# Optimization experiments

Hardware: AMD Instinct MI355X
Metric: run time of the kernel (lower is better)

Reference implementation:

```python
import jax, jax.numpy as jnp
import numpy as np

B, S, D = 2, 2048, 2048          # batch, seq_len, model_dim
H, HD, RD, L = 16, 128, 64, 512  # heads, head_dim, rope_dim, latent_dim


def _rope_cos_sin(seq_len, dim, dtype):
    inv_freq = 1.0 / (10000.0 ** (jnp.arange(0, dim, 2, dtype=jnp.float32) / dim))
    freqs = jnp.outer(jnp.arange(seq_len, dtype=jnp.float32), inv_freq)  # [S, dim/2]
    emb = jnp.concatenate([freqs, freqs], axis=-1)                        # [S, dim]
    return jnp.cos(emb).astype(dtype), jnp.sin(emb).astype(dtype)


def _rotate_half(x):
    x1, x2 = jnp.split(x, 2, axis=-1)
    return jnp.concatenate([-x2, x1], axis=-1)


def _apply_rope(q, k):
    # q, k: [B, S, H, rope_dim]
    cos, sin = _rope_cos_sin(q.shape[1], q.shape[-1], q.dtype)
    cos = cos[None, :, None, :]
    sin = sin[None, :, None, :]
    return q * cos + _rotate_half(q) * sin, k * cos + _rotate_half(k) * sin


def setup_inputs() -> dict:
    key = jax.random.key(0)
    ks = jax.random.split(key, 6)
    x = jax.random.normal(ks[0], (B, S, D), dtype=jnp.float32)
    mask = jnp.tril(jnp.ones((1, 1, S, S), dtype=jnp.bool_))  # causal
    s = lambda fan_in: 1.0 / np.sqrt(fan_in)
    w_kv_down = jax.random.normal(ks[1], (D, L), jnp.float32) * s(D)
    w_kv_up = jax.random.normal(ks[2], (L, H * (2 * HD + RD)), jnp.float32) * s(L)
    w_q_down = jax.random.normal(ks[3], (D, L), jnp.float32) * s(D)
    w_q_up = jax.random.normal(ks[4], (L, H * (HD + RD)), jnp.float32) * s(L)
    w_o = jax.random.normal(ks[5], (H * HD, D), jnp.float32) * s(H * HD)
    return dict(x=x, mask=mask, w_kv_down=w_kv_down, w_kv_up=w_kv_up,
                w_q_down=w_q_down, w_q_up=w_q_up, w_o=w_o)


def reference(x, mask, w_kv_down, w_kv_up, w_q_down, w_q_up, w_o):
    b, s, _ = x.shape
    # low-rank KV path
    kv_full = (x @ w_kv_down @ w_kv_up).reshape(b, s, H, 2 * HD + RD)
    k_content = kv_full[..., :HD]
    k_rope = kv_full[..., HD:HD + RD]
    v = kv_full[..., HD + RD:]                     # [b, s, H, HD]
    # low-rank Q path
    q_full = (x @ w_q_down @ w_q_up).reshape(b, s, H, HD + RD)
    q_content = q_full[..., :HD]
    q_rope = q_full[..., HD:]
    # partial RoPE on the rope slice only
    q_rope, k_rope = _apply_rope(q_rope, k_rope)
    q = jnp.concatenate([q_content, q_rope], axis=-1)  # [b, s, H, HD+RD]
    k = jnp.concatenate([k_content, k_rope], axis=-1)
    scale = 1.0 / np.sqrt(HD + RD)
    scores = jnp.einsum('bqhd,bkhd->bhqk', q, k) * scale
    scores = jnp.where(mask, scores, jnp.finfo(scores.dtype).min)
    attn = jax.nn.softmax(scores, axis=-1)          # dropout_p=0.0 -> identity
    context = jnp.einsum('bhqk,bkhd->bqhd', attn, v).reshape(b, s, H * HD)
    return context @ w_o
```

## Files before the change

### kernel.cpp

```cpp
#include <hip/hip_runtime.h>
#include <hip/hip_bf16.h>

#define B_ 2
#define S_ 2048
#define D_ 2048
#define H_ 16
#define HD_ 128
#define RD_ 64
#define L_ 512
#define BS_ (B_ * S_)
#define KVH 320
#define QH 192

typedef unsigned short u16;
typedef __bf16 bf16x8 __attribute__((ext_vector_type(8)));
typedef float f32x4 __attribute__((ext_vector_type(4)));
typedef unsigned short us8 __attribute__((ext_vector_type(8)));
typedef unsigned short us4 __attribute__((ext_vector_type(4)));

#define MFMA16(A, B, C) __builtin_amdgcn_mfma_f32_16x16x32_bf16((A), (B), (C), 0, 0, 0)

__device__ __forceinline__ u16 f2bf(float f) {
    unsigned int u = __builtin_bit_cast(unsigned int, f);
    u += 0x7FFFu + ((u >> 16) & 1u);
    return (u16)(u >> 16);
}
__device__ __forceinline__ float bf2f(u16 u) {
    unsigned int x = ((unsigned int)u) << 16;
    return __builtin_bit_cast(float, x);
}
__device__ __forceinline__ void async16(const void* g, void* l) {
    __builtin_amdgcn_global_load_lds((void __attribute__((address_space(1)))*)g,
                                     (void __attribute__((address_space(3)))*)l, 16, 0, 0);
}
__device__ __forceinline__ int swz4(int row) { return (row + (row >> 2)) & 3; }

__global__ __launch_bounds__(256) void conv_f32_bf16(const float* __restrict__ in,
                                                     u16* __restrict__ outp) {
    const int i = blockIdx.x * 256 + threadIdx.x;
    float4 v = *(const float4*)(in + (size_t)i * 4);
    us4 o; o[0] = f2bf(v.x); o[1] = f2bf(v.y); o[2] = f2bf(v.z); o[3] = f2bf(v.w);
    *(us4*)(outp + (size_t)i * 4) = o;
}

__global__ __launch_bounds__(256) void transpose_f32_bf16(const float* __restrict__ W,
                                                          u16* __restrict__ Wt,
                                                          int K, int N) {
    __shared__ float tile[32][33];
    const int t = threadIdx.x, tx = t & 31, ty = t >> 5;
    const int n0 = blockIdx.x * 32, k0 = blockIdx.y * 32;
#pragma unroll
    for (int r = 0; r < 4; r++)
        tile[ty + 8 * r][tx] = W[(size_t)(k0 + ty + 8 * r) * N + n0 + tx];
    __syncthreads();
#pragma unroll
    for (int r = 0; r < 4; r++)
        Wt[(size_t)(n0 + ty + 8 * r) * K + k0 + tx] = f2bf(tile[tx][ty + 8 * r]);
}

__global__ __launch_bounds__(256) void transpose_v(const u16* __restrict__ kvf,
                                                   u16* __restrict__ vtg) {
    __shared__ u16 tile[32][33];
    const int t = threadIdx.x, tx = t & 31, ty = t >> 5;
    const int bh = blockIdx.z, b = bh >> 4, h = bh & 15;
    const int s0 = blockIdx.x * 32, d0 = blockIdx.y * 32;
#pragma unroll
    for (int r = 0; r < 4; r++)
        tile[ty + 8 * r][tx] = kvf[(size_t)(b * S_ + s0 + ty + 8 * r) * (H_ * KVH) + h * KVH + QH + d0 + tx];
    __syncthreads();
#pragma unroll
    for (int r = 0; r < 4; r++)
        vtg[((size_t)bh * HD_ + d0 + ty + 8 * r) * S_ + s0 + tx] = tile[tx][ty + 8 * r];
}

__global__ __launch_bounds__(256) void rope_both(u16* __restrict__ qf,
                                                 u16* __restrict__ kvf) {
    const int idx = blockIdx.x * 256 + threadIdx.x;
    const int d = idx & 31;
    const int h = (idx >> 5) & (H_ - 1);
    const int s = (idx >> 9) & (S_ - 1);
    const int b = idx >> 20;
    const int stride = blockIdx.y ? KVH : QH;
    u16* buf = blockIdx.y ? kvf : qf;

    const float inv_freq = powf(10000.0f, -(float)d * (1.0f / 32.0f));
    const float ang = (float)s * inv_freq;
    const float c = cosf(ang), sn = sinf(ang);

    u16* p = buf + ((size_t)((b * S_ + s) * H_) + h) * stride + HD_ + d;
    const float x1 = bf2f(p[0]);
    const float x2 = bf2f(p[32]);
    p[0]  = f2bf(x1 * c - x2 * sn);
    p[32] = f2bf(x2 * c + x1 * sn);
}

template <int WM, int WN, int TM, int TN, bool OUT_F32>
__global__ __launch_bounds__(WM * WN * 64) void gemm_bf16(
    const u16* __restrict__ A, int lda,
    const u16* __restrict__ Bt, int ldb,
    void* __restrict__ Cv, int ldc, int K) {
    constexpr int BMt = WM * TM * 16;
    constexpr int BNt = WN * TN * 16;
    constexpr int NW  = WM * WN;
    constexpr int CA  = BMt / 16;
    constexpr int CB  = BNt / 16;

    __shared__ u16 As[BMt * 32];
    __shared__ u16 Bs[BNt * 32];

    const int t = threadIdx.x, w = t >> 6, l = t & 63;
    const int quad = l >> 4, n16 = l & 15;
    const int wr = w / WN, wc = w % WN;
    const size_t m0 = (size_t)blockIdx.y * BMt;
    const size_t n0 = (size_t)blockIdx.x * BNt;
    const int rowc = l >> 2, sbp = l & 3;

    f32x4 acc[TM][TN];
#pragma unroll
    for (int i = 0; i < TM; i++)
#pragma unroll
        for (int j = 0; j < TN; j++) acc[i][j] = (f32x4){0.f, 0.f, 0.f, 0.f};

    for (int k0 = 0; k0 < K; k0 += 32) {
#pragma unroll
        for (int c = w; c < CA; c += NW) {
            const int row = c * 16 + rowc;
            const int colc = ((sbp - swz4(row)) & 3) * 8;
            async16(A + (m0 + row) * lda + k0 + colc, &As[c * 512 + l * 8]);
        }
#pragma unroll
        for (int c = w; c < CB; c += NW) {
            const int row = c * 16 + rowc;
            const int colc = ((sbp - swz4(row)) & 3) * 8;
            async16(Bt + (n0 + row) * ldb + k0 + colc, &Bs[c * 512 + l * 8]);
        }
        __syncthreads();

        bf16x8 af[TM], bfr[TN];
#pragma unroll
        for (int i = 0; i < TM; i++) {
            const int row = wr * TM * 16 + i * 16 + n16;
            af[i] = *(const bf16x8*)&As[row * 32 + ((quad + swz4(row)) & 3) * 8];
        }
#pragma unroll
        for (int j = 0; j < TN; j++) {
            const int row = wc * TN * 16 + j * 16 + n16;
            bfr[j] = *(const bf16x8*)&Bs[row * 32 + ((quad + swz4(row)) & 3) * 8];
        }
#pragma unroll
        for (int i = 0; i < TM; i++)
#pragma unroll
            for (int j = 0; j < TN; j++) acc[i][j] = MFMA16(af[i], bfr[j], acc[i][j]);
        __syncthreads();
    }

#pragma unroll
    for (int i = 0; i < TM; i++) {
#pragma unroll
        for (int j = 0; j < TN; j++) {
#pragma unroll
            for (int r = 0; r < 4; r++) {
                const size_t row = m0 + wr * TM * 16 + i * 16 + quad * 4 + r;
                const size_t col = n0 + wc * TN * 16 + j * 16 + n16;
                if (OUT_F32) ((float*)Cv)[row * ldc + col] = acc[i][j][r];
                else         ((u16*)Cv)[row * ldc + col] = f2bf(acc[i][j][r]);
            }
        }
    }
}

#define PS_STRIDE 72

__global__ __launch_bounds__(256) void attn_mfma(const u16* __restrict__ qf,
                                                 const u16* __restrict__ kvf,
                                                 const u16* __restrict__ vtg,
                                                 u16* __restrict__ ctx) {
    __shared__ u16 Ks[6 * 2048];
    __shared__ u16 Vs[2 * 4096];
    __shared__ u16 Ps[4][16 * PS_STRIDE];

    const int t = threadIdx.x, w = t >> 6, lane = t & 63;
    const int quad = lane >> 4, n16 = lane & 15;
    const int bh = blockIdx.y, b = bh >> 4, h = bh & 15;
    const int q0 = (S_ / 64 - 1 - (int)blockIdx.x) * 64;

    const float sc2 = 1.442695041f / 13.856406461f;

    const u16* Kbase = kvf + (size_t)(b * S_) * (H_ * KVH) + h * KVH;
    const u16* Vbase = vtg + (size_t)bh * HD_ * S_;

    const int srow = lane >> 2;
    const int sbp  = lane & 3;

    bf16x8 qfrag[6];
    {
        const u16* qr = qf + (size_t)(b * S_ + q0 + w * 16 + n16) * (H_ * QH) + h * QH + quad * 8;
#pragma unroll
        for (int c = 0; c < 6; c++) qfrag[c] = *(const bf16x8*)(qr + c * 32);
    }

    f32x4 O[8];
#pragma unroll
    for (int i = 0; i < 8; i++) O[i] = (f32x4){0.f, 0.f, 0.f, 0.f};
    float lrun[4] = {0.f, 0.f, 0.f, 0.f};

    const int nkt = q0 / 64 + 1;
    for (int kt = 0; kt < nkt; kt++) {
        const int kb = kt * 64;

#pragma unroll
        for (int i = w; i < 24; i += 4) {
            const int c = i >> 2, g = i & 3;
            const int row = g * 16 + srow;
            const int colc = ((sbp - swz4(row)) & 3) * 8;
            async16(Kbase + (size_t)(kb + row) * (H_ * KVH) + c * 32 + colc,
                    &Ks[c * 2048 + g * 512 + lane * 8]);
        }
#pragma unroll
        for (int i = w; i < 16; i += 4) {
            const int c2 = i >> 3, g = i & 7;
            const int dim = g * 16 + srow;
            const int colc = ((sbp - swz4(dim)) & 3) * 8;
            async16(Vbase + (size_t)dim * S_ + kb + c2 * 32 + colc,
                    &Vs[c2 * 4096 + g * 512 + lane * 8]);
        }
        __syncthreads();

        float Sv[4][4];
#pragma unroll
        for (int nt = 0; nt < 4; nt++) {
            const int row = nt * 16 + n16;
            f32x4 s = (f32x4){0.f, 0.f, 0.f, 0.f};
#pragma unroll
            for (int c = 0; c < 6; c++) {
                bf16x8 kf = *(const bf16x8*)&Ks[c * 2048 + row * 32 + ((quad + swz4(row)) & 3) * 8];
                s = MFMA16(qfrag[c], kf, s);
            }
#pragma unroll
            for (int r = 0; r < 4; r++) Sv[nt][r] = s[r];
        }
        if (kb == q0) {
#pragma unroll
            for (int nt = 0; nt < 4; nt++)
#pragma unroll
                for (int r = 0; r < 4; r++)
                    if (nt * 16 + n16 > w * 16 + quad * 4 + r) Sv[nt][r] = -1.0e30f;
        }

#pragma unroll
        for (int nt = 0; nt < 4; nt++)
#pragma unroll
            for (int r = 0; r < 4; r++) {
                const float p = exp2f(Sv[nt][r] * sc2);
                lrun[r] += p;
                Ps[w][(quad * 4 + r) * PS_STRIDE + nt * 16 + n16] = f2bf(p);
            }

#pragma unroll
        for (int c2 = 0; c2 < 2; c2++) {
            bf16x8 pf = *(const bf16x8*)&Ps[w][n16 * PS_STRIDE + c2 * 32 + quad * 8];
#pragma unroll
            for (int nt = 0; nt < 8; nt++) {
                const int row = nt * 16 + n16;
                bf16x8 vf = *(const bf16x8*)&Vs[c2 * 4096 + row * 32 + ((quad + swz4(row)) & 3) * 8];
                O[nt] = MFMA16(pf, vf, O[nt]);
            }
        }
        __syncthreads();
    }

#pragma unroll
    for (int off = 1; off < 16; off <<= 1)
#pragma unroll
        for (int r = 0; r < 4; r++) lrun[r] += __shfl_xor(lrun[r], off, 64);

    float inv[4];
#pragma unroll
    for (int r = 0; r < 4; r++) inv[r] = 1.0f / lrun[r];
#pragma unroll
    for (int nt = 0; nt < 8; nt++)
#pragma unroll
        for (int r = 0; r < 4; r++) {
            const int qrow = q0 + w * 16 + quad * 4 + r;
            ctx[(size_t)(b * S_ + qrow) * (H_ * HD_) + h * HD_ + nt * 16 + n16] =
                f2bf(O[nt][r] * inv[r]);
        }
}

extern "C" void kernel_launch(void* const* d_in, const int* in_sizes, int n_in,
                              void* d_out, int out_size, void* d_ws, size_t ws_size,
                              hipStream_t stream) {
    const float* x         = (const float*)d_in[0];
    const float* w_kv_down = (const float*)d_in[2];
    const float* w_kv_up   = (const float*)d_in[3];
    const float* w_q_down  = (const float*)d_in[4];
    const float* w_q_up    = (const float*)d_in[5];
    const float* w_o       = (const float*)d_in[6];
    float* out = (float*)d_out;

    char* ws = (char*)d_ws;
    size_t off = 0;
    u16* xb      = (u16*)(ws + off); off += (size_t)BS_ * D_ * 2;
    u16* wdt     = (u16*)(ws + off); off += (size_t)1024 * D_ * 2;
    u16* wkvup_t = (u16*)(ws + off); off += (size_t)(H_ * KVH) * L_ * 2;
    u16* wqup_t  = (u16*)(ws + off); off += (size_t)(H_ * QH) * L_ * 2;
    u16* wo_t    = (u16*)(ws + off); off += (size_t)D_ * (H_ * HD_) * 2;
    u16* low     = (u16*)(ws + off); off += (size_t)BS_ * 1024 * 2;
    u16* kv_full = (u16*)(ws + off); off += (size_t)BS_ * H_ * KVH * 2;
    u16* q_full  = (u16*)(ws + off); off += (size_t)BS_ * H_ * QH * 2;
    u16* vtg     = (u16*)(ws + off); off += (size_t)B_ * H_ * HD_ * S_ * 2;
    u16* ctx     = (u16*)(ws + off); off += (size_t)BS_ * H_ * HD_ * 2;

    conv_f32_bf16<<<(BS_ * D_) / 1024, 256, 0, stream>>>(x, xb);
    transpose_f32_bf16<<<dim3(L_ / 32, D_ / 32), 256, 0, stream>>>(w_kv_down, wdt, D_, L_);
    transpose_f32_bf16<<<dim3(L_ / 32, D_ / 32), 256, 0, stream>>>(w_q_down, wdt + (size_t)512 * D_, D_, L_);
    transpose_f32_bf16<<<dim3((H_ * KVH) / 32, L_ / 32), 256, 0, stream>>>(w_kv_up, wkvup_t, L_, H_ * KVH);
    transpose_f32_bf16<<<dim3((H_ * QH) / 32, L_ / 32), 256, 0, stream>>>(w_q_up, wqup_t, L_, H_ * QH);
    transpose_f32_bf16<<<dim3(D_ / 32, (H_ * HD_) / 32), 256, 0, stream>>>(w_o, wo_t, H_ * HD_, D_);

    gemm_bf16<2, 2, 4, 2, false><<<dim3(1024 / 64, BS_ / 128), 256, 0, stream>>>(
        xb, D_, wdt, D_, low, 1024, D_);
    gemm_bf16<2, 2, 4, 4, false><<<dim3((H_ * KVH) / 128, BS_ / 128), 256, 0, stream>>>(
        low, 1024, wkvup_t, L_, kv_full, H_ * KVH, L_);
    gemm_bf16<2, 2, 4, 4, false><<<dim3((H_ * QH) / 128, BS_ / 128), 256, 0, stream>>>(
        low + 512, 1024, wqup_t, L_, q_full, H_ * QH, L_);

    rope_both<<<dim3((B_ * S_ * H_ * 32) / 256, 2), 256, 0, stream>>>(q_full, kv_full);

    transpose_v<<<dim3(S_ / 32, HD_ / 32, B_ * H_), 256, 0, stream>>>(kv_full, vtg);

    attn_mfma<<<dim3(S_ / 64, B_ * H_), 256, 0, stream>>>(q_full, kv_full, vtg, ctx);

    gemm_bf16<2, 2, 4, 4, true><<<dim3(D_ / 128, BS_ / 128), 256, 0, stream>>>(
        ctx, D_, wo_t, D_, out, D_, D_);
}
```

Baseline: 468.1 us.

## Double-buffer K tiles with async prefetch and transpose score MFMA layout

Double-buffers the K shared-memory tile so the next tile's K loads are issued while the current tile is computed. V loads are issued after a barrier and waited on separately with explicit vmcnt counts. The score MFMA operands are swapped so each lane holds a column of probabilities, which allows packed 4-wide writes of P to shared memory and a single per-lane running sum with a cheaper reduction. This adds shared memory usage and relies on hand-counted waitcnt values that must match the number of outstanding loads.

```diff
diff --git a/kernel.cpp b/kernel.cpp
--- a/kernel.cpp
+++ b/kernel.cpp
@@ -169,15 +169,15 @@
     }
 }
 
-#define PS_STRIDE 72
+#define PST 88
 
 __global__ __launch_bounds__(256) void attn_mfma(const u16* __restrict__ qf,
                                                  const u16* __restrict__ kvf,
                                                  const u16* __restrict__ vtg,
                                                  u16* __restrict__ ctx) {
-    __shared__ u16 Ks[6 * 2048];
+    __shared__ u16 Ks[2][6 * 2048];
     __shared__ u16 Vs[2 * 4096];
-    __shared__ u16 Ps[4][16 * PS_STRIDE];
+    __shared__ u16 Ps[4][16 * PST];
 
     const int t = threadIdx.x, w = t >> 6, lane = t & 63;
     const int quad = lane >> 4, n16 = lane & 15;
@@ -202,29 +202,45 @@
     f32x4 O[8];
 #pragma unroll
     for (int i = 0; i < 8; i++) O[i] = (f32x4){0.f, 0.f, 0.f, 0.f};
-    float lrun[4] = {0.f, 0.f, 0.f, 0.f};
+    float lrun = 0.f;
 
     const int nkt = q0 / 64 + 1;
+
+#define ISSUE_K(KT, BUF)                                                          \
+    _Pragma("unroll")                                                             \
+    for (int i = w; i < 24; i += 4) {                                             \
+        const int c = i >> 2, g = i & 3;                                          \
+        const int row = g * 16 + srow;                                            \
+        const int colc = ((sbp - swz4(row)) & 3) * 8;                             \
+        async16(Kbase + (size_t)((KT) * 64 + row) * (H_ * KVH) + c * 32 + colc,   \
+                &Ks[BUF][c * 2048 + g * 512 + lane * 8]);                         \
+    }
+#define ISSUE_V(KT)                                                               \
+    _Pragma("unroll")                                                             \
+    for (int i = w; i < 16; i += 4) {                                             \
+        const int c2 = i >> 3, g = i & 7;                                         \
+        const int dim = g * 16 + srow;                                            \
+        const int colc = ((sbp - swz4(dim)) & 3) * 8;                             \
+        async16(Vbase + (size_t)dim * S_ + (KT) * 64 + c2 * 32 + colc,            \
+                &Vs[c2 * 4096 + g * 512 + lane * 8]);                             \
+    }
+
+    ISSUE_K(0, 0);
+    ISSUE_V(0);
+
     for (int kt = 0; kt < nkt; kt++) {
-        const int kb = kt * 64;
-
-#pragma unroll
-        for (int i = w; i < 24; i += 4) {
-            const int c = i >> 2, g = i & 3;
-            const int row = g * 16 + srow;
-            const int colc = ((sbp - swz4(row)) & 3) * 8;
-            async16(Kbase + (size_t)(kb + row) * (H_ * KVH) + c * 32 + colc,
-                    &Ks[c * 2048 + g * 512 + lane * 8]);
-        }
-#pragma unroll
-        for (int i = w; i < 16; i += 4) {
-            const int c2 = i >> 3, g = i & 7;
-            const int dim = g * 16 + srow;
-            const int colc = ((sbp - swz4(dim)) & 3) * 8;
-            async16(Vbase + (size_t)dim * S_ + kb + c2 * 32 + colc,
-                    &Vs[c2 * 4096 + g * 512 + lane * 8]);
-        }
-        __syncthreads();
+        const int cur = kt & 1;
+        if (kt > 0) {
+            asm volatile("s_barrier" ::: "memory");
+            ISSUE_V(kt);
+        }
+        if (kt + 1 < nkt) {
+            ISSUE_K(kt + 1, cur ^ 1);
+            asm volatile("s_waitcnt vmcnt(10)" ::: "memory");
+        } else {
+            asm volatile("s_waitcnt vmcnt(4)" ::: "memory");
+        }
+        asm volatile("s_barrier" ::: "memory");
 
         float Sv[4][4];
 #pragma unroll
@@ -233,32 +249,39 @@
             f32x4 s = (f32x4){0.f, 0.f, 0.f, 0.f};
 #pragma unroll
             for (int c = 0; c < 6; c++) {
-                bf16x8 kf = *(const bf16x8*)&Ks[c * 2048 + row * 32 + ((quad + swz4(row)) & 3) * 8];
-                s = MFMA16(qfrag[c], kf, s);
+                bf16x8 kf = *(const bf16x8*)&Ks[cur][c * 2048 + row * 32 + ((quad + swz4(row)) & 3) * 8];
+                s = MFMA16(kf, qfrag[c], s);
             }
 #pragma unroll
             for (int r = 0; r < 4; r++) Sv[nt][r] = s[r];
         }
-        if (kb == q0) {
+        if (kt * 64 == q0) {
 #pragma unroll
             for (int nt = 0; nt < 4; nt++)
 #pragma unroll
                 for (int r = 0; r < 4; r++)
-                    if (nt * 16 + n16 > w * 16 + quad * 4 + r) Sv[nt][r] = -1.0e30f;
-        }
-
-#pragma unroll
-        for (int nt = 0; nt < 4; nt++)
+                    if (nt * 16 + 4 * quad + r > w * 16 + n16) Sv[nt][r] = -1.0e30f;
+        }
+
+#pragma unroll
+        for (int nt = 0; nt < 4; nt++) {
+            us4 pk;
 #pragma unroll
             for (int r = 0; r < 4; r++) {
                 const float p = exp2f(Sv[nt][r] * sc2);
-                lrun[r] += p;
-                Ps[w][(quad * 4 + r) * PS_STRIDE + nt * 16 + n16] = f2bf(p);
+                lrun += p;
+                pk[r] = f2bf(p);
             }
+            *(us4*)&Ps[w][n16 * PST + nt * 16 + 4 * quad] = pk;
+        }
+
+        if (kt + 1 < nkt) asm volatile("s_waitcnt vmcnt(6)" ::: "memory");
+        else              asm volatile("s_waitcnt vmcnt(0)" ::: "memory");
+        asm volatile("s_barrier" ::: "memory");
 
 #pragma unroll
         for (int c2 = 0; c2 < 2; c2++) {
-            bf16x8 pf = *(const bf16x8*)&Ps[w][n16 * PS_STRIDE + c2 * 32 + quad * 8];
+            bf16x8 pf = *(const bf16x8*)&Ps[w][n16 * PST + c2 * 32 + 8 * quad];
 #pragma unroll
             for (int nt = 0; nt < 8; nt++) {
                 const int row = nt * 16 + n16;
@@ -266,17 +289,15 @@
                 O[nt] = MFMA16(pf, vf, O[nt]);
             }
         }
-        __syncthreads();
-    }
-
-#pragma unroll
-    for (int off = 1; off < 16; off <<= 1)
-#pragma unroll
-        for (int r = 0; r < 4; r++) lrun[r] += __shfl_xor(lrun[r], off, 64);
+    }
+
+    lrun += __shfl_xor(lrun, 16, 64);
+    lrun += __shfl_xor(lrun, 32, 64);
 
     float inv[4];
 #pragma unroll
-    for (int r = 0; r < 4; r++) inv[r] = 1.0f / lrun[r];
+    for (int r = 0; r < 4; r++) inv[r] = 1.0f / __shfl(lrun, 4 * quad + r, 64);
+
 #pragma unroll
     for (int nt = 0; nt < 8; nt++)
 #pragma unroll
```

Result: faster. 450.9 us (-3.7%).

## Use 32x32 MFMA with 128-row query tiles in attention and merge weight transposes

Applied to the files above, without the earlier changes.

The attention kernel now gives each block 128 query rows, 32 per wave, and uses the 32x32x16 bf16 MFMA in place of the 16x16x32 one. Each K/V tile loaded into LDS is therefore shared by twice as many queries. Scores are computed as K·Q so each lane holds one query column, and waves whose queries lie entirely before a key tile skip it. The five weight-transpose launches are also merged into one kernel to cut launch overhead. In exchange, the LDS swizzle is dropped, which risks bank conflicts, and the grid has fewer, longer blocks, which changes causal load balance.

```diff
diff --git a/kernel.cpp b/kernel.cpp
--- a/kernel.cpp
+++ b/kernel.cpp
@@ -15,10 +15,11 @@
 typedef unsigned short u16;
 typedef __bf16 bf16x8 __attribute__((ext_vector_type(8)));
 typedef float f32x4 __attribute__((ext_vector_type(4)));
-typedef unsigned short us8 __attribute__((ext_vector_type(8)));
+typedef float f32x16 __attribute__((ext_vector_type(16)));
 typedef unsigned short us4 __attribute__((ext_vector_type(4)));
 
 #define MFMA16(A, B, C) __builtin_amdgcn_mfma_f32_16x16x32_bf16((A), (B), (C), 0, 0, 0)
+#define MFMA32(A, B, C) __builtin_amdgcn_mfma_f32_32x32x16_bf16((A), (B), (C), 0, 0, 0)
 
 __device__ __forceinline__ u16 f2bf(float f) {
     unsigned int u = __builtin_bit_cast(unsigned int, f);
@@ -43,12 +44,23 @@
     *(us4*)(outp + (size_t)i * 4) = o;
 }
 
-__global__ __launch_bounds__(256) void transpose_f32_bf16(const float* __restrict__ W,
-                                                          u16* __restrict__ Wt,
-                                                          int K, int N) {
+__global__ __launch_bounds__(256) void prep_weights(
+    const float* __restrict__ w_kv_down, const float* __restrict__ w_q_down,
+    const float* __restrict__ w_kv_up,   const float* __restrict__ w_q_up,
+    const float* __restrict__ w_o,
+    u16* __restrict__ wdt, u16* __restrict__ wkvup_t,
+    u16* __restrict__ wqup_t, u16* __restrict__ wo_t) {
     __shared__ float tile[32][33];
+    const int blk = blockIdx.x;
+    const float* W; u16* Wt; int K, N, bx, by;
+    if (blk < 1024)      { W = w_kv_down; Wt = wdt;                      K = 2048; N = 512;  int r = blk;        bx = r & 15;  by = r >> 4; }
+    else if (blk < 2048) { W = w_q_down;  Wt = wdt + (size_t)512 * 2048; K = 2048; N = 512;  int r = blk - 1024; bx = r & 15;  by = r >> 4; }
+    else if (blk < 4608) { W = w_kv_up;   Wt = wkvup_t;                  K = 512;  N = 5120; int r = blk - 2048; bx = r % 160; by = r / 160; }
+    else if (blk < 6144) { W = w_q_up;    Wt = wqup_t;                   K = 512;  N = 3072; int r = blk - 4608; bx = r % 96;  by = r / 96; }
+    else                 { W = w_o;       Wt = wo_t;                     K = 2048; N = 2048; int r = blk - 6144; bx = r & 63;  by = r >> 6; }
+
     const int t = threadIdx.x, tx = t & 31, ty = t >> 5;
-    const int n0 = blockIdx.x * 32, k0 = blockIdx.y * 32;
+    const int n0 = bx * 32, k0 = by * 32;
 #pragma unroll
     for (int r = 0; r < 4; r++)
         tile[ty + 8 * r][tx] = W[(size_t)(k0 + ty + 8 * r) * N + n0 + tx];
@@ -169,122 +181,120 @@
     }
 }
 
-#define PS_STRIDE 72
+#define PST32 72
 
 __global__ __launch_bounds__(256) void attn_mfma(const u16* __restrict__ qf,
                                                  const u16* __restrict__ kvf,
                                                  const u16* __restrict__ vtg,
                                                  u16* __restrict__ ctx) {
-    __shared__ u16 Ks[6 * 2048];
-    __shared__ u16 Vs[2 * 4096];
-    __shared__ u16 Ps[4][16 * PS_STRIDE];
+    __shared__ u16 Ks[12 * 1024];
+    __shared__ u16 Vs[4 * 2048];
+    __shared__ u16 Ps[4][32 * PST32];
 
     const int t = threadIdx.x, w = t >> 6, lane = t & 63;
-    const int quad = lane >> 4, n16 = lane & 15;
-    const int bh = blockIdx.y, b = bh >> 4, h = bh & 15;
-    const int q0 = (S_ / 64 - 1 - (int)blockIdx.x) * 64;
+    const int h = lane >> 5, l31 = lane & 31;
+    const int bh = blockIdx.y, b = bh >> 4, hd = bh & 15;
+    const int q0 = (15 - (int)blockIdx.x) * 128;
+    const int q0w = q0 + 32 * w;
 
     const float sc2 = 1.442695041f / 13.856406461f;
 
-    const u16* Kbase = kvf + (size_t)(b * S_) * (H_ * KVH) + h * KVH;
+    const u16* Kbase = kvf + (size_t)(b * S_) * (H_ * KVH) + hd * KVH;
     const u16* Vbase = vtg + (size_t)bh * HD_ * S_;
 
-    const int srow = lane >> 2;
-    const int sbp  = lane & 3;
-
-    bf16x8 qfrag[6];
+    bf16x8 qfrag[12];
     {
-        const u16* qr = qf + (size_t)(b * S_ + q0 + w * 16 + n16) * (H_ * QH) + h * QH + quad * 8;
-#pragma unroll
-        for (int c = 0; c < 6; c++) qfrag[c] = *(const bf16x8*)(qr + c * 32);
-    }
-
-    f32x4 O[8];
-#pragma unroll
-    for (int i = 0; i < 8; i++) O[i] = (f32x4){0.f, 0.f, 0.f, 0.f};
-    float lrun[4] = {0.f, 0.f, 0.f, 0.f};
-
-    const int nkt = q0 / 64 + 1;
+        const u16* qr = qf + (size_t)(b * S_ + q0w + l31) * (H_ * QH) + hd * QH;
+#pragma unroll
+        for (int kc = 0; kc < 12; kc++) qfrag[kc] = *(const bf16x8*)(qr + kc * 16 + h * 8);
+    }
+
+    f32x16 O[4];
+#pragma unroll
+    for (int dg = 0; dg < 4; dg++)
+#pragma unroll
+        for (int i = 0; i < 16; i++) O[dg][i] = 0.f;
+    float lrun = 0.f;
+
+    const int nkt = q0 / 64 + 2;
     for (int kt = 0; kt < nkt; kt++) {
         const int kb = kt * 64;
 
 #pragma unroll
         for (int i = w; i < 24; i += 4) {
-            const int c = i >> 2, g = i & 3;
-            const int row = g * 16 + srow;
-            const int colc = ((sbp - swz4(row)) & 3) * 8;
-            async16(Kbase + (size_t)(kb + row) * (H_ * KVH) + c * 32 + colc,
-                    &Ks[c * 2048 + g * 512 + lane * 8]);
+            const int kc = i % 12, g = i / 12;
+            const int row = g * 32 + (lane >> 1);
+            async16(Kbase + (size_t)(kb + row) * (H_ * KVH) + kc * 16 + (lane & 1) * 8,
+                    &Ks[kc * 1024 + g * 512 + lane * 8]);
         }
 #pragma unroll
         for (int i = w; i < 16; i += 4) {
-            const int c2 = i >> 3, g = i & 7;
-            const int dim = g * 16 + srow;
-            const int colc = ((sbp - swz4(dim)) & 3) * 8;
-            async16(Vbase + (size_t)dim * S_ + kb + c2 * 32 + colc,
-                    &Vs[c2 * 4096 + g * 512 + lane * 8]);
+            const int kc = i >> 2, dg = i & 3;
+            const int d = dg * 32 + (lane >> 1);
+            async16(Vbase + (size_t)d * S_ + kb + kc * 16 + (lane & 1) * 8,
+                    &Vs[kc * 2048 + dg * 512 + lane * 8]);
         }
         __syncthreads();
 
-        float Sv[4][4];
-#pragma unroll
-        for (int nt = 0; nt < 4; nt++) {
-            const int row = nt * 16 + n16;
-            f32x4 s = (f32x4){0.f, 0.f, 0.f, 0.f};
-#pragma unroll
-            for (int c = 0; c < 6; c++) {
-                bf16x8 kf = *(const bf16x8*)&Ks[c * 2048 + row * 32 + ((quad + swz4(row)) & 3) * 8];
-                s = MFMA16(qfrag[c], kf, s);
+        const bool skip = kb > q0w + 31;
+        if (!skip) {
+            f32x16 Sa[2];
+#pragma unroll
+            for (int mg = 0; mg < 2; mg++) {
+#pragma unroll
+                for (int i = 0; i < 16; i++) Sa[mg][i] = 0.f;
+#pragma unroll
+                for (int kc = 0; kc < 12; kc++) {
+                    bf16x8 kf = *(const bf16x8*)&Ks[kc * 1024 + (mg * 32 + l31) * 16 + h * 8];
+                    Sa[mg] = MFMA32(kf, qfrag[kc], Sa[mg]);
+                }
             }
-#pragma unroll
-            for (int r = 0; r < 4; r++) Sv[nt][r] = s[r];
-        }
-        if (kb == q0) {
-#pragma unroll
-            for (int nt = 0; nt < 4; nt++)
-#pragma unroll
-                for (int r = 0; r < 4; r++)
-                    if (nt * 16 + n16 > w * 16 + quad * 4 + r) Sv[nt][r] = -1.0e30f;
-        }
-
-#pragma unroll
-        for (int nt = 0; nt < 4; nt++)
-#pragma unroll
-            for (int r = 0; r < 4; r++) {
-                const float p = exp2f(Sv[nt][r] * sc2);
-                lrun[r] += p;
-                Ps[w][(quad * 4 + r) * PS_STRIDE + nt * 16 + n16] = f2bf(p);
+
+            const bool partial = (kb + 63 > q0w);
+            const int q = q0w + l31;
+#pragma unroll
+            for (int mg = 0; mg < 2; mg++) {
+#pragma unroll
+                for (int g = 0; g < 4; g++) {
+                    us4 pk;
+#pragma unroll
+                    for (int rr = 0; rr < 4; rr++) {
+                        const int kpos = kb + mg * 32 + 8 * g + 4 * h + rr;
+                        float s = Sa[mg][g * 4 + rr];
+                        if (partial && kpos > q) s = -1.0e30f;
+                        const float p = exp2f(s * sc2);
+                        lrun += p;
+                        pk[rr] = f2bf(p);
+                    }
+                    *(us4*)&Ps[w][l31 * PST32 + mg * 32 + 8 * g + 4 * h] = pk;
+                }
             }
 
 #pragma unroll
-        for (int c2 = 0; c2 < 2; c2++) {
-            bf16x8 pf = *(const bf16x8*)&Ps[w][n16 * PS_STRIDE + c2 * 32 + quad * 8];
-#pragma unroll
-            for (int nt = 0; nt < 8; nt++) {
-                const int row = nt * 16 + n16;
-                bf16x8 vf = *(const bf16x8*)&Vs[c2 * 4096 + row * 32 + ((quad + swz4(row)) & 3) * 8];
-                O[nt] = MFMA16(pf, vf, O[nt]);
+            for (int kc = 0; kc < 4; kc++) {
+                bf16x8 pf = *(const bf16x8*)&Ps[w][l31 * PST32 + kc * 16 + h * 8];
+#pragma unroll
+                for (int dg = 0; dg < 4; dg++) {
+                    bf16x8 vf = *(const bf16x8*)&Vs[kc * 2048 + (dg * 32 + l31) * 16 + h * 8];
+                    O[dg] = MFMA32(pf, vf, O[dg]);
+                }
             }
         }
         __syncthreads();
     }
 
-#pragma unroll
-    for (int off = 1; off < 16; off <<= 1)
-#pragma unroll
-        for (int r = 0; r < 4; r++) lrun[r] += __shfl_xor(lrun[r], off, 64);
-
-    float inv[4];
-#pragma unroll
-    for (int r = 0; r < 4; r++) inv[r] = 1.0f / lrun[r];
-#pragma unroll
-    for (int nt = 0; nt < 8; nt++)
-#pragma unroll
-        for (int r = 0; r < 4; r++) {
-            const int qrow = q0 + w * 16 + quad * 4 + r;
-            ctx[(size_t)(b * S_ + qrow) * (H_ * HD_) + h * HD_ + nt * 16 + n16] =
-                f2bf(O[nt][r] * inv[r]);
-        }
+    lrun += __shfl_xor(lrun, 32, 64);
+    const float invq = 1.0f / lrun;
+
+#pragma unroll
+    for (int reg = 0; reg < 16; reg++) {
+        const int qoff = (reg & 3) + 8 * (reg >> 2) + 4 * h;
+        const float vinv = __shfl(invq, qoff, 64);
+        u16* crow = ctx + (size_t)(b * S_ + q0w + qoff) * (H_ * HD_) + hd * HD_;
+#pragma unroll
+        for (int dg = 0; dg < 4; dg++)
+            crow[dg * 32 + l31] = f2bf(O[dg][reg] * vinv);
+    }
 }
 
 extern "C" void kernel_launch(void* const* d_in, const int* in_sizes, int n_in,
@@ -312,11 +322,8 @@
     u16* ctx     = (u16*)(ws + off); off += (size_t)BS_ * H_ * HD_ * 2;
 
     conv_f32_bf16<<<(BS_ * D_) / 1024, 256, 0, stream>>>(x, xb);
-    transpose_f32_bf16<<<dim3(L_ / 32, D_ / 32), 256, 0, stream>>>(w_kv_down, wdt, D_, L_);
-    transpose_f32_bf16<<<dim3(L_ / 32, D_ / 32), 256, 0, stream>>>(w_q_down, wdt + (size_t)512 * D_, D_, L_);
-    transpose_f32_bf16<<<dim3((H_ * KVH) / 32, L_ / 32), 256, 0, stream>>>(w_kv_up, wkvup_t, L_, H_ * KVH);
-    transpose_f32_bf16<<<dim3((H_ * QH) / 32, L_ / 32), 256, 0, stream>>>(w_q_up, wqup_t, L_, H_ * QH);
-    transpose_f32_bf16<<<dim3(D_ / 32, (H_ * HD_) / 32), 256, 0, stream>>>(w_o, wo_t, H_ * HD_, D_);
+    prep_weights<<<10240, 256, 0, stream>>>(w_kv_down, w_q_down, w_kv_up, w_q_up, w_o,
+                                            wdt, wkvup_t, wqup_t, wo_t);
 
     gemm_bf16<2, 2, 4, 2, false><<<dim3(1024 / 64, BS_ / 128), 256, 0, stream>>>(
         xb, D_, wdt, D_, low, 1024, D_);
@@ -329,7 +336,7 @@
 
     transpose_v<<<dim3(S_ / 32, HD_ / 32, B_ * H_), 256, 0, stream>>>(kv_full, vtg);
 
-    attn_mfma<<<dim3(S_ / 64, B_ * H_), 256, 0, stream>>>(q_full, kv_full, vtg, ctx);
+    attn_mfma<<<dim3(S_ / 128, B_ * H_), 256, 0, stream>>>(q_full, kv_full, vtg, ctx);
 
     gemm_bf16<2, 2, 4, 4, true><<<dim3(D_ / 128, BS_ / 128), 256, 0, stream>>>(
         ctx, D_, wo_t, D_, out, D_, D_);
```

Measured after the change: 498.4 us. 6.5% more time.
